# Kernel tuning notes

Hardware: AMD Instinct MI355X
Metric: run time of the kernel (lower is better)

Reference implementation:

```python
import jax, jax.numpy as jnp
import numpy as np

NUM_HEADS = 8
LN_EPS = 1e-5  # torch.nn.LayerNorm default


def setup_inputs() -> dict:
    key = jax.random.key(0)
    k1, k2, k3, k4 = jax.random.split(key, 4)
    B, S, H = 32, 512, 256
    inputs = jax.random.normal(k1, (B, S, H), dtype=jnp.float32)
    radial_mask = jax.random.uniform(k2, (B, S), dtype=jnp.float32, minval=1e-4, maxval=1.0)
    # torch Linear stores weight as [out, in]; init ~ U(-1/sqrt(in), 1/sqrt(in))
    bound = 1.0 / np.sqrt(H)
    in_proj_w = jax.random.uniform(k3, (3 * H, H), dtype=jnp.float32, minval=-bound, maxval=bound)
    out_proj_w = jax.random.uniform(k4, (H, H), dtype=jnp.float32, minval=-bound, maxval=bound)
    ln_gamma = jnp.ones((H,), dtype=jnp.float32)
    ln_beta = jnp.zeros((H,), dtype=jnp.float32)
    return {
        "inputs": inputs,
        "radial_mask": radial_mask,
        "in_proj_w": in_proj_w,
        "out_proj_w": out_proj_w,
        "ln_gamma": ln_gamma,
        "ln_beta": ln_beta,
    }


def reference(inputs, radial_mask, in_proj_w, out_proj_w, ln_gamma, ln_beta):
    B, S, H = inputs.shape
    nh = NUM_HEADS
    hd = H // nh

    # LayerNorm over the last dim
    mu = jnp.mean(inputs, axis=-1, keepdims=True)
    var = jnp.var(inputs, axis=-1, keepdims=True)
    normed = (inputs - mu) * jax.lax.rsqrt(var + LN_EPS) * ln_gamma + ln_beta

    # QKV projection (no bias); torch Linear: x @ W.T
    qkv = jnp.einsum('bsh,oh->bso', normed, in_proj_w)
    q, k, v = jnp.split(qkv, 3, axis=-1)

    # [B, S, H] -> [B, nh, S, hd]
    def to_heads(x):
        return x.reshape(B, S, nh, hd).transpose(0, 2, 1, 3)

    q = to_heads(q)
    k = to_heads(k)
    v = to_heads(v)

    # Custom transforms before SDPA
    q = q * q + 1e-6
    k = k + jnp.log(radial_mask)[:, None, :, None]

    # scaled_dot_product_attention with default scale = 1/sqrt(hd)
    scale = 1.0 / np.sqrt(hd).astype(np.float32)
    scores = jnp.einsum('bhqd,bhkd->bhqk', q, k) * scale
    attn = jax.nn.softmax(scores, axis=-1)
    out = jnp.einsum('bhqk,bhkd->bhqd', attn, v)

    # back to [B, S, H], output projection, residual with 1/sqrt(2)
    out = out.transpose(0, 2, 1, 3).reshape(B, S, H)
    out = jnp.einsum('bsh,oh->bso', out, out_proj_w)
    return (out + inputs) * np.float32(0.5 ** 0.5)
```

## Files before the change

kernel.cpp:

```cpp
#include <hip/hip_runtime.h>
#include <hip/hip_bf16.h>

typedef unsigned int u32;
typedef unsigned short u16;

#define B_   32
#define S_   512
#define H_   256
#define NH_  8
#define HD_  32

typedef __attribute__((ext_vector_type(8))) short short8;
typedef __attribute__((ext_vector_type(4))) float f32x4;

__device__ __forceinline__ float bfl(u32 u){ union{u32 i;float f;} c; c.i = u << 16;          return c.f; }
__device__ __forceinline__ float bfh(u32 u){ union{u32 i;float f;} c; c.i = u & 0xffff0000u;  return c.f; }
__device__ __forceinline__ float bf1(u16 u){ union{u32 i;float f;} c; c.i = ((u32)u) << 16;   return c.f; }
__device__ __forceinline__ u16   f2b(float f){ __hip_bfloat16 h = __float2bfloat16(f); return *reinterpret_cast<u16*>(&h); }
__device__ __forceinline__ u32   pk2(float a, float b){ return (u32)f2b(a) | ((u32)f2b(b) << 16); }
__device__ __forceinline__ void  unp8(const uint4 u, float* f){
  f[0]=bfl(u.x); f[1]=bfh(u.x); f[2]=bfl(u.y); f[3]=bfh(u.y);
  f[4]=bfl(u.z); f[5]=bfh(u.z); f[6]=bfl(u.w); f[7]=bfh(u.w);
}
__device__ __forceinline__ f32x4 mfma16(short8 a, short8 b, f32x4 c){
  return __builtin_amdgcn_mfma_f32_16x16x32_bf16(a, b, c, 0, 0, 0);
}

template<int F32>
__device__ __forceinline__ void load8(const void* p, int e8, float* f) {
  if (F32) {
    const float4* q = (const float4*)p;
    const float4 a = q[e8 * 2], b = q[e8 * 2 + 1];
    f[0]=a.x; f[1]=a.y; f[2]=a.z; f[3]=a.w; f[4]=b.x; f[5]=b.y; f[6]=b.z; f[7]=b.w;
  } else {
    unp8(((const uint4*)p)[e8], f);
  }
}
template<int F32>
__device__ __forceinline__ void store8(void* p, int e8, const float* f) {
  if (F32) {
    float4* q = (float4*)p;
    q[e8 * 2]     = make_float4(f[0], f[1], f[2], f[3]);
    q[e8 * 2 + 1] = make_float4(f[4], f[5], f[6], f[7]);
  } else {
    uint4 u;
    u.x = pk2(f[0], f[1]); u.y = pk2(f[2], f[3]);
    u.z = pk2(f[4], f[5]); u.w = pk2(f[6], f[7]);
    ((uint4*)p)[e8] = u;
  }
}
template<int F32>
__device__ __forceinline__ float load1(const void* p, size_t e) {
  return F32 ? ((const float*)p)[e] : bf1(((const u16*)p)[e]);
}
template<int F32>
__device__ __forceinline__ short8 loadBfrag(const void* wp, int row, int k0, int K) {
  if (F32) {
    const float* w = (const float*)wp + (size_t)row * K + k0;
    const float4 a = *(const float4*)w;
    const float4 b = *(const float4*)(w + 4);
    short8 r;
    r[0]=(short)f2b(a.x); r[1]=(short)f2b(a.y); r[2]=(short)f2b(a.z); r[3]=(short)f2b(a.w);
    r[4]=(short)f2b(b.x); r[5]=(short)f2b(b.y); r[6]=(short)f2b(b.z); r[7]=(short)f2b(b.w);
    return r;
  } else {
    return *(const short8*)((const u16*)wp + (size_t)row * K + k0);
  }
}

__device__ __forceinline__ int sniff_mode(const void* xin) {
  __shared__ int votes;
  const int tid = threadIdx.x;
  if (tid == 0) votes = 0;
  __syncthreads();
  const u32* xw = (const u32*)xin;
  int h = 0;
#pragma unroll
  for (int j = 0; j < 4; ++j) {
    const u32 u = xw[(tid << 2) + j];
    const u32 e = (u >> 7) & 0xFF;
    h += (e >= 100 && e <= 135) ? 1 : 0;
  }
  const unsigned long long m = __ballot(h >= 3);
  if ((tid & 63) == 0) atomicAdd(&votes, __popcll(m));
  __syncthreads();
  return (votes >= 128) ? 0 : 1;
}

template<int F32>
__global__ __launch_bounds__(256, 2) void ln_qkv_mfma(
    const void* __restrict__ xin, const void* __restrict__ rmask,
    const void* __restrict__ wi, const void* __restrict__ gamma,
    const void* __restrict__ beta,
    u16* __restrict__ qbuf, u16* __restrict__ kbuf, u16* __restrict__ vt)
{
  if (sniff_mode(xin) != F32) return;

  __shared__ __align__(16) u16 XnF[4 * 8 * 64 * 8];
  __shared__ float lmr[64];
  const int tid = threadIdx.x;
  const int l = tid & 63, w = tid >> 6;
  const int lr = l & 15, quad = l >> 4;
  const int row0 = (blockIdx.x >> 1) * 64;
  const int nhalf = blockIdx.x & 1;

  {
    const int r = tid >> 5, ln = tid & 31;
    float g[8], bb[8];
    load8<F32>(gamma, ln, g);
    load8<F32>(beta,  ln, bb);
    const int c = ln >> 2, qd = ln & 3;
#pragma unroll
    for (int p = 0; p < 8; ++p) {
      const int R = p * 8 + r;
      const int grow = row0 + R;
      float x[8]; load8<F32>(xin, grow * 32 + ln, x);
      float s = 0.f, sq = 0.f;
#pragma unroll
      for (int j = 0; j < 8; ++j) { s += x[j]; sq += x[j] * x[j]; }
#pragma unroll
      for (int m = 1; m < 32; m <<= 1) { s += __shfl_xor(s, m); sq += __shfl_xor(sq, m); }
      const float mu  = s * (1.f / 256.f);
      const float var = sq * (1.f / 256.f) - mu * mu;
      const float rs  = rsqrtf(var + 1e-5f);
      short8 pk;
#pragma unroll
      for (int j = 0; j < 8; ++j) pk[j] = (short)f2b((x[j] - mu) * rs * g[j] + bb[j]);
      const int t = R >> 4, rm = R & 15;
      *(short8*)(XnF + (((t * 8 + c) * 64 + qd * 16 + rm) << 3)) = pk;
      if (ln == 0) lmr[R] = logf(load1<F32>(rmask, grow));
    }
  }
  __syncthreads();

  short8 Af[4][8];
#pragma unroll
  for (int mt = 0; mt < 4; ++mt)
#pragma unroll
    for (int c = 0; c < 8; ++c)
      Af[mt][c] = *(const short8*)(XnF + (((mt * 8 + c) * 64 + l) << 3));

  const int bb_ = row0 >> 9;
  const int sB  = row0 & 511;
  const int tbase = nhalf * 24 + w * 6;

  short8 Bf[2][8];
#pragma unroll
  for (int c = 0; c < 8; ++c)
    Bf[0][c] = loadBfrag<F32>(wi, tbase * 16 + lr, c * 32 + quad * 8, 256);

#pragma unroll
  for (int nt = 0; nt < 6; ++nt) {
    const int cb = nt & 1;
    if (nt < 5) {
#pragma unroll
      for (int c = 0; c < 8; ++c)
        Bf[cb ^ 1][c] = loadBfrag<F32>(wi, (tbase + nt + 1) * 16 + lr, c * 32 + quad * 8, 256);
    }

    f32x4 a[4];
#pragma unroll
    for (int mt = 0; mt < 4; ++mt) a[mt] = (f32x4){0.f, 0.f, 0.f, 0.f};
#pragma unroll
    for (int c = 0; c < 8; ++c) {
#pragma unroll
      for (int mt = 0; mt < 4; ++mt)
        a[mt] = mfma16(Af[mt][c], Bf[cb][c], a[mt]);
    }

    const int nAbs  = (tbase + nt) * 16;
    const int type  = nAbs >> 8;
    const int dbase = nAbs & 255;
    if (type < 2) {
      const int d  = dbase + lr;
      const int h  = d >> 5, dd = d & 31;
      const int bh = bb_ * NH_ + h;
      u16* dst = (type == 0) ? qbuf : kbuf;
#pragma unroll
      for (int mt = 0; mt < 4; ++mt) {
        const int sL = mt * 16 + quad * 4;
#pragma unroll
        for (int i = 0; i < 4; ++i) {
          float v = a[mt][i];
          v = (type == 0) ? (v * v + 1e-6f) : (v + lmr[sL + i]);
          dst[((size_t)bh * S_ + sB + sL + i) * HD_ + dd] = f2b(v);
        }
      }
    } else {
      const int dv  = dbase + lr;
      const int hv  = dv >> 5, ddv = dv & 31;
      const int bhv = bb_ * NH_ + hv;
#pragma unroll
      for (int mt = 0; mt < 4; ++mt) {
        const int c16 = (sB >> 5) + (mt >> 1);
        const int slot16 = ((c16 * 2 + (ddv >> 4)) * 4 + quad) * 16 + (ddv & 15);
        uint2 pkv;
        pkv.x = pk2(a[mt][0], a[mt][1]);
        pkv.y = pk2(a[mt][2], a[mt][3]);
        *(uint2*)(vt + (size_t)bhv * (S_ * HD_) + slot16 * 8 + (mt & 1) * 4) = pkv;
      }
    }
  }
}

__global__ __launch_bounds__(256, 4) void attn_mfma(
    const u16* __restrict__ qbuf, const u16* __restrict__ kbuf,
    const u16* __restrict__ vt, u16* __restrict__ ctx)
{
  __shared__ __align__(16) u16 OB[4][16 * 40];
  const int tid = threadIdx.x;
  const int bh = blockIdx.x & 255, sq = blockIdx.x >> 8;
  const int l = tid & 63, w = tid >> 6;
  const int lr = l & 15, quad = l >> 4;
  const size_t kvbase = (size_t)bh * (S_ * HD_);
  const int q0 = sq * 64 + w * 16;

  const float cE = 0.17677669529663688f * 1.4426950408889634f;

  const short8 qf = *(const short8*)(qbuf + kvbase + (size_t)(q0 + lr) * HD_ + quad * 8);
  const u16* kp = kbuf + kvbase + (size_t)lr * HD_ + quad * 8;
  const u16* vp = vt + kvbase;

  float mS = -1e30f, lS = 0.f;
  f32x4 o0 = {0.f,0.f,0.f,0.f}, o1 = {0.f,0.f,0.f,0.f};

#pragma unroll
  for (int c = 0; c < 4; ++c) {
    f32x4 acc[8];
#pragma unroll
    for (int j = 0; j < 8; ++j) {
      const short8 kf = *(const short8*)(kp + (c * 8 + j) * (16 * HD_));
      f32x4 z = {0.f,0.f,0.f,0.f};
      acc[j] = mfma16(kf, qf, z);
    }

    float mc = acc[0][0];
#pragma unroll
    for (int j = 0; j < 8; ++j)
#pragma unroll
      for (int r = 0; r < 4; ++r) mc = fmaxf(mc, acc[j][r]);
    mc = fmaxf(mc, __shfl_xor(mc, 16));
    mc = fmaxf(mc, __shfl_xor(mc, 32));
    const float mNew  = fmaxf(mS, mc * cE);
    const float alpha = exp2f(mS - mNew);
    float sc = 0.f;
#pragma unroll
    for (int j = 0; j < 8; ++j)
#pragma unroll
      for (int r = 0; r < 4; ++r) {
        const float p = exp2f(fmaf(acc[j][r], cE, -mNew));
        acc[j][r] = p; sc += p;
      }
    sc += __shfl_xor(sc, 16);
    sc += __shfl_xor(sc, 32);
    lS = fmaf(lS, alpha, sc);
    mS = mNew;
#pragma unroll
    for (int r = 0; r < 4; ++r) { o0[r] *= alpha; o1[r] *= alpha; }

#pragma unroll
    for (int g = 0; g < 4; ++g) {
      union { u32 u[4]; short8 s; } pa;
      pa.u[0] = pk2(acc[2*g][0],   acc[2*g][1]);
      pa.u[1] = pk2(acc[2*g][2],   acc[2*g][3]);
      pa.u[2] = pk2(acc[2*g+1][0], acc[2*g+1][1]);
      pa.u[3] = pk2(acc[2*g+1][2], acc[2*g+1][3]);
      const int c16 = c * 4 + g;
      const short8 v0 = *(const short8*)(vp + (((c16 * 8 +     quad) * 16 + lr) << 3));
      const short8 v1 = *(const short8*)(vp + (((c16 * 8 + 4 + quad) * 16 + lr) << 3));
      o0 = mfma16(pa.s, v0, o0);
      o1 = mfma16(pa.s, v1, o1);
    }
  }
  const float inv = 1.f / lS;

  u16* ob = OB[w];
#pragma unroll
  for (int r = 0; r < 4; ++r) {
    const int qq = quad * 4 + r;
    const float iv = __shfl(inv, (l & 48) | qq);
    ob[qq * 40 + lr]      = f2b(o0[r] * iv);
    ob[qq * 40 + 16 + lr] = f2b(o1[r] * iv);
  }
  const uint4 ov = *(const uint4*)(ob + (l >> 2) * 40 + (l & 3) * 8);
  *(uint4*)(ctx + kvbase + (size_t)(q0 + (l >> 2)) * HD_ + (l & 3) * 8) = ov;
}

template<int F32>
__global__ __launch_bounds__(256) void proj_mfma(
    const u16* __restrict__ ctx, const void* __restrict__ xin,
    const void* __restrict__ wo, void* __restrict__ out)
{
  if (sniff_mode(xin) != F32) return;

  __shared__ __align__(16) u16 XnF[8 * 64 * 8];
  __shared__ __align__(16) u16 OutB[16 * 264];
  const int tid = threadIdx.x;
  const int l = tid & 63, w = tid >> 6;
  const int lr = l & 15, quad = l >> 4;
  const int row0 = blockIdx.x * 16;
  const int b = row0 >> 9, s0 = row0 & 511;

#pragma unroll
  for (int it = 0; it < 2; ++it) {
    const int idx = it * 256 + tid;
    const int dq = idx & 3, sl = (idx >> 2) & 15, h = idx >> 6;
    const uint4 cv = *(const uint4*)(ctx + ((size_t)(b * 8 + h) * S_ + s0 + sl) * HD_ + dq * 8);
    const int qds = dq ^ (sl & 3);
    *(uint4*)(XnF + ((h * 64 + qds * 16 + sl) << 3)) = cv;
  }
  __syncthreads();

  const int lsw = (quad ^ (lr & 3)) * 16 + lr;
  short8 Af[8];
#pragma unroll
  for (int c = 0; c < 8; ++c)
    Af[c] = *(const short8*)(XnF + ((c * 64 + lsw) << 3));

  short8 Bf[2][8];
#pragma unroll
  for (int c = 0; c < 8; ++c)
    Bf[0][c] = loadBfrag<F32>(wo, (w * 4) * 16 + lr, c * 32 + quad * 8, 256);

#pragma unroll
  for (int nt = 0; nt < 4; ++nt) {
    const int cb = nt & 1;
    if (nt < 3) {
#pragma unroll
      for (int c = 0; c < 8; ++c)
        Bf[cb ^ 1][c] = loadBfrag<F32>(wo, (w * 4 + nt + 1) * 16 + lr, c * 32 + quad * 8, 256);
    }
    const int n0 = (w * 4 + nt) * 16;
    f32x4 a0 = {0.f,0.f,0.f,0.f};
#pragma unroll
    for (int c = 0; c < 8; ++c)
      a0 = mfma16(Af[c], Bf[cb][c], a0);
#pragma unroll
    for (int i = 0; i < 4; ++i)
      OutB[(quad * 4 + i) * 264 + n0 + lr] = f2b(a0[i]);
  }
  __syncthreads();

  const int r  = tid >> 4;
  const int c8 = (tid & 15) * 2;
#pragma unroll
  for (int j8 = 0; j8 < 2; ++j8) {
    float xv[8]; load8<F32>(xin, (row0 + r) * 32 + c8 + j8, xv);
    float pv[8]; unp8(*(const uint4*)(OutB + r * 264 + (c8 + j8) * 8), pv);
    float ov[8];
#pragma unroll
    for (int j = 0; j < 8; ++j) ov[j] = (pv[j] + xv[j]) * 0.70710678f;
    store8<F32>(out, (row0 + r) * 32 + c8 + j8, ov);
  }
}

extern "C" void kernel_launch(void* const* d_in, const int* in_sizes, int n_in,
                              void* d_out, int out_size, void* d_ws, size_t ws_size,
                              hipStream_t stream)
{
  const void* xin   = d_in[0];
  const void* rmask = d_in[1];
  const void* wi    = d_in[2];
  const void* wo    = d_in[3];
  const void* gam   = d_in[4];
  const void* bet   = d_in[5];

  u16* q   = (u16*)d_ws;
  u16* k   = q + 4194304;
  u16* vt  = k + 4194304;
  u16* cxb = vt + 4194304;

  ln_qkv_mfma<0><<<512,  256, 0, stream>>>(xin, rmask, wi, gam, bet, q, k, vt);
  ln_qkv_mfma<1><<<512,  256, 0, stream>>>(xin, rmask, wi, gam, bet, q, k, vt);
  attn_mfma     <<<2048, 256, 0, stream>>>(q, k, vt, cxb);
  proj_mfma<0>  <<<1024, 256, 0, stream>>>(cxb, xin, wo, d_out);
  proj_mfma<1>  <<<1024, 256, 0, stream>>>(cxb, xin, wo, d_out);
}
```

Before: 181.0 us.

## Double per-wave query rows in attention and rows per block in output projection

The attention kernel now has each wave process two 16-row query tiles (32 rows), so every loaded K and V fragment feeds two sets of MFMAs, and the grid is halved. The output projection block now covers 32 rows instead of 16, reusing each loaded Wo fragment for two M-tiles, and its grid is also halved. This cuts redundant K/V and weight traffic per unit of work. In exchange it raises register pressure (the launch bounds are lowered to 3 and 2 waves) and leaves fewer blocks for latency hiding.

```diff
diff --git a/kernel.cpp b/kernel.cpp
--- a/kernel.cpp
+++ b/kernel.cpp
@@ -203,119 +203,143 @@
   }
 }
 
-__global__ __launch_bounds__(256, 4) void attn_mfma(
+__global__ __launch_bounds__(256, 3) void attn_mfma(
     const u16* __restrict__ qbuf, const u16* __restrict__ kbuf,
     const u16* __restrict__ vt, u16* __restrict__ ctx)
 {
-  __shared__ __align__(16) u16 OB[4][16 * 40];
+  __shared__ __align__(16) u16 OB[4][32 * 40];
   const int tid = threadIdx.x;
   const int bh = blockIdx.x & 255, sq = blockIdx.x >> 8;
   const int l = tid & 63, w = tid >> 6;
   const int lr = l & 15, quad = l >> 4;
   const size_t kvbase = (size_t)bh * (S_ * HD_);
-  const int q0 = sq * 64 + w * 16;
+  const int q0 = sq * 128 + w * 32;
 
   const float cE = 0.17677669529663688f * 1.4426950408889634f;
 
-  const short8 qf = *(const short8*)(qbuf + kvbase + (size_t)(q0 + lr) * HD_ + quad * 8);
+  const short8 qfA = *(const short8*)(qbuf + kvbase + (size_t)(q0 + lr) * HD_ + quad * 8);
+  const short8 qfB = *(const short8*)(qbuf + kvbase + (size_t)(q0 + 16 + lr) * HD_ + quad * 8);
   const u16* kp = kbuf + kvbase + (size_t)lr * HD_ + quad * 8;
   const u16* vp = vt + kvbase;
 
-  float mS = -1e30f, lS = 0.f;
-  f32x4 o0 = {0.f,0.f,0.f,0.f}, o1 = {0.f,0.f,0.f,0.f};
+  float mSA = -1e30f, lSA = 0.f, mSB = -1e30f, lSB = 0.f;
+  f32x4 oA0 = {0.f,0.f,0.f,0.f}, oA1 = {0.f,0.f,0.f,0.f};
+  f32x4 oB0 = {0.f,0.f,0.f,0.f}, oB1 = {0.f,0.f,0.f,0.f};
 
 #pragma unroll
   for (int c = 0; c < 4; ++c) {
-    f32x4 acc[8];
+    f32x4 aA[8], aB[8];
 #pragma unroll
     for (int j = 0; j < 8; ++j) {
       const short8 kf = *(const short8*)(kp + (c * 8 + j) * (16 * HD_));
       f32x4 z = {0.f,0.f,0.f,0.f};
-      acc[j] = mfma16(kf, qf, z);
-    }
-
-    float mc = acc[0][0];
+      aA[j] = mfma16(kf, qfA, z);
+      aB[j] = mfma16(kf, qfB, z);
+    }
+
+    float mcA = aA[0][0], mcB = aB[0][0];
 #pragma unroll
     for (int j = 0; j < 8; ++j)
 #pragma unroll
-      for (int r = 0; r < 4; ++r) mc = fmaxf(mc, acc[j][r]);
-    mc = fmaxf(mc, __shfl_xor(mc, 16));
-    mc = fmaxf(mc, __shfl_xor(mc, 32));
-    const float mNew  = fmaxf(mS, mc * cE);
-    const float alpha = exp2f(mS - mNew);
-    float sc = 0.f;
+      for (int r = 0; r < 4; ++r) { mcA = fmaxf(mcA, aA[j][r]); mcB = fmaxf(mcB, aB[j][r]); }
+    mcA = fmaxf(mcA, __shfl_xor(mcA, 16)); mcB = fmaxf(mcB, __shfl_xor(mcB, 16));
+    mcA = fmaxf(mcA, __shfl_xor(mcA, 32)); mcB = fmaxf(mcB, __shfl_xor(mcB, 32));
+    const float mNA = fmaxf(mSA, mcA * cE), mNB = fmaxf(mSB, mcB * cE);
+    const float alA = exp2f(mSA - mNA),     alB = exp2f(mSB - mNB);
+    float scA = 0.f, scB = 0.f;
 #pragma unroll
     for (int j = 0; j < 8; ++j)
 #pragma unroll
       for (int r = 0; r < 4; ++r) {
-        const float p = exp2f(fmaf(acc[j][r], cE, -mNew));
-        acc[j][r] = p; sc += p;
+        const float pA = exp2f(fmaf(aA[j][r], cE, -mNA));
+        const float pB = exp2f(fmaf(aB[j][r], cE, -mNB));
+        aA[j][r] = pA; scA += pA;
+        aB[j][r] = pB; scB += pB;
       }
-    sc += __shfl_xor(sc, 16);
-    sc += __shfl_xor(sc, 32);
-    lS = fmaf(lS, alpha, sc);
-    mS = mNew;
-#pragma unroll
-    for (int r = 0; r < 4; ++r) { o0[r] *= alpha; o1[r] *= alpha; }
+    scA += __shfl_xor(scA, 16); scB += __shfl_xor(scB, 16);
+    scA += __shfl_xor(scA, 32); scB += __shfl_xor(scB, 32);
+    lSA = fmaf(lSA, alA, scA); mSA = mNA;
+    lSB = fmaf(lSB, alB, scB); mSB = mNB;
+#pragma unroll
+    for (int r = 0; r < 4; ++r) {
+      oA0[r] *= alA; oA1[r] *= alA;
+      oB0[r] *= alB; oB1[r] *= alB;
+    }
 
 #pragma unroll
     for (int g = 0; g < 4; ++g) {
-      union { u32 u[4]; short8 s; } pa;
-      pa.u[0] = pk2(acc[2*g][0],   acc[2*g][1]);
-      pa.u[1] = pk2(acc[2*g][2],   acc[2*g][3]);
-      pa.u[2] = pk2(acc[2*g+1][0], acc[2*g+1][1]);
-      pa.u[3] = pk2(acc[2*g+1][2], acc[2*g+1][3]);
       const int c16 = c * 4 + g;
       const short8 v0 = *(const short8*)(vp + (((c16 * 8 +     quad) * 16 + lr) << 3));
       const short8 v1 = *(const short8*)(vp + (((c16 * 8 + 4 + quad) * 16 + lr) << 3));
-      o0 = mfma16(pa.s, v0, o0);
-      o1 = mfma16(pa.s, v1, o1);
-    }
-  }
-  const float inv = 1.f / lS;
+      union { u32 u[4]; short8 s; } pa;
+      pa.u[0] = pk2(aA[2*g][0],   aA[2*g][1]);
+      pa.u[1] = pk2(aA[2*g][2],   aA[2*g][3]);
+      pa.u[2] = pk2(aA[2*g+1][0], aA[2*g+1][1]);
+      pa.u[3] = pk2(aA[2*g+1][2], aA[2*g+1][3]);
+      oA0 = mfma16(pa.s, v0, oA0);
+      oA1 = mfma16(pa.s, v1, oA1);
+      pa.u[0] = pk2(aB[2*g][0],   aB[2*g][1]);
+      pa.u[1] = pk2(aB[2*g][2],   aB[2*g][3]);
+      pa.u[2] = pk2(aB[2*g+1][0], aB[2*g+1][1]);
+      pa.u[3] = pk2(aB[2*g+1][2], aB[2*g+1][3]);
+      oB0 = mfma16(pa.s, v0, oB0);
+      oB1 = mfma16(pa.s, v1, oB1);
+    }
+  }
+  const float invA = 1.f / lSA, invB = 1.f / lSB;
 
   u16* ob = OB[w];
 #pragma unroll
   for (int r = 0; r < 4; ++r) {
     const int qq = quad * 4 + r;
-    const float iv = __shfl(inv, (l & 48) | qq);
-    ob[qq * 40 + lr]      = f2b(o0[r] * iv);
-    ob[qq * 40 + 16 + lr] = f2b(o1[r] * iv);
-  }
-  const uint4 ov = *(const uint4*)(ob + (l >> 2) * 40 + (l & 3) * 8);
-  *(uint4*)(ctx + kvbase + (size_t)(q0 + (l >> 2)) * HD_ + (l & 3) * 8) = ov;
-}
-
-template<int F32>
-__global__ __launch_bounds__(256) void proj_mfma(
+    const float ivA = __shfl(invA, (l & 48) | qq);
+    const float ivB = __shfl(invB, (l & 48) | qq);
+    ob[qq * 40 + lr]             = f2b(oA0[r] * ivA);
+    ob[qq * 40 + 16 + lr]        = f2b(oA1[r] * ivA);
+    ob[(16 + qq) * 40 + lr]      = f2b(oB0[r] * ivB);
+    ob[(16 + qq) * 40 + 16 + lr] = f2b(oB1[r] * ivB);
+  }
+#pragma unroll
+  for (int t = 0; t < 2; ++t) {
+    const int row = (l >> 2) + t * 16;
+    const uint4 ov = *(const uint4*)(ob + row * 40 + (l & 3) * 8);
+    *(uint4*)(ctx + kvbase + (size_t)(q0 + row) * HD_ + (l & 3) * 8) = ov;
+  }
+}
+
+template<int F32>
+__global__ __launch_bounds__(256, 2) void proj_mfma(
     const u16* __restrict__ ctx, const void* __restrict__ xin,
     const void* __restrict__ wo, void* __restrict__ out)
 {
   if (sniff_mode(xin) != F32) return;
 
-  __shared__ __align__(16) u16 XnF[8 * 64 * 8];
-  __shared__ __align__(16) u16 OutB[16 * 264];
+  __shared__ __align__(16) u16 XnF[2 * 8 * 64 * 8];
+  __shared__ __align__(16) u16 OutB[32 * 264];
   const int tid = threadIdx.x;
   const int l = tid & 63, w = tid >> 6;
   const int lr = l & 15, quad = l >> 4;
-  const int row0 = blockIdx.x * 16;
+  const int row0 = blockIdx.x * 32;
   const int b = row0 >> 9, s0 = row0 & 511;
 
 #pragma unroll
-  for (int it = 0; it < 2; ++it) {
+  for (int it = 0; it < 4; ++it) {
     const int idx = it * 256 + tid;
-    const int dq = idx & 3, sl = (idx >> 2) & 15, h = idx >> 6;
+    const int dq = idx & 3, sl = (idx >> 2) & 31, h = idx >> 7;
     const uint4 cv = *(const uint4*)(ctx + ((size_t)(b * 8 + h) * S_ + s0 + sl) * HD_ + dq * 8);
-    const int qds = dq ^ (sl & 3);
-    *(uint4*)(XnF + ((h * 64 + qds * 16 + sl) << 3)) = cv;
+    const int t = sl >> 4, rm = sl & 15;
+    const int qds = dq ^ (rm & 3);
+    *(uint4*)(XnF + (((t * 8 + h) * 64 + qds * 16 + rm) << 3)) = cv;
   }
   __syncthreads();
 
   const int lsw = (quad ^ (lr & 3)) * 16 + lr;
-  short8 Af[8];
-#pragma unroll
-  for (int c = 0; c < 8; ++c)
-    Af[c] = *(const short8*)(XnF + ((c * 64 + lsw) << 3));
+  short8 Af[2][8];
+#pragma unroll
+  for (int mt = 0; mt < 2; ++mt)
+#pragma unroll
+    for (int c = 0; c < 8; ++c)
+      Af[mt][c] = *(const short8*)(XnF + (((mt * 8 + c) * 64 + lsw) << 3));
 
   short8 Bf[2][8];
 #pragma unroll
@@ -331,20 +355,26 @@
         Bf[cb ^ 1][c] = loadBfrag<F32>(wo, (w * 4 + nt + 1) * 16 + lr, c * 32 + quad * 8, 256);
     }
     const int n0 = (w * 4 + nt) * 16;
-    f32x4 a0 = {0.f,0.f,0.f,0.f};
-#pragma unroll
-    for (int c = 0; c < 8; ++c)
-      a0 = mfma16(Af[c], Bf[cb][c], a0);
-#pragma unroll
-    for (int i = 0; i < 4; ++i)
-      OutB[(quad * 4 + i) * 264 + n0 + lr] = f2b(a0[i]);
+    f32x4 a0 = {0.f,0.f,0.f,0.f}, a1 = {0.f,0.f,0.f,0.f};
+#pragma unroll
+    for (int c = 0; c < 8; ++c) {
+      a0 = mfma16(Af[0][c], Bf[cb][c], a0);
+      a1 = mfma16(Af[1][c], Bf[cb][c], a1);
+    }
+#pragma unroll
+    for (int m = 0; m < 2; ++m) {
+      const f32x4 acc = m ? a1 : a0;
+#pragma unroll
+      for (int i = 0; i < 4; ++i)
+        OutB[(m * 16 + quad * 4 + i) * 264 + n0 + lr] = f2b(acc[i]);
+    }
   }
   __syncthreads();
 
-  const int r  = tid >> 4;
-  const int c8 = (tid & 15) * 2;
-#pragma unroll
-  for (int j8 = 0; j8 < 2; ++j8) {
+  const int r  = tid >> 3;
+  const int c8 = (tid & 7) * 4;
+#pragma unroll
+  for (int j8 = 0; j8 < 4; ++j8) {
     float xv[8]; load8<F32>(xin, (row0 + r) * 32 + c8 + j8, xv);
     float pv[8]; unp8(*(const uint4*)(OutB + r * 264 + (c8 + j8) * 8), pv);
     float ov[8];
@@ -372,7 +402,7 @@
 
   ln_qkv_mfma<0><<<512,  256, 0, stream>>>(xin, rmask, wi, gam, bet, q, k, vt);
   ln_qkv_mfma<1><<<512,  256, 0, stream>>>(xin, rmask, wi, gam, bet, q, k, vt);
-  attn_mfma     <<<2048, 256, 0, stream>>>(q, k, vt, cxb);
-  proj_mfma<0>  <<<1024, 256, 0, stream>>>(cxb, xin, wo, d_out);
-  proj_mfma<1>  <<<1024, 256, 0, stream>>>(cxb, xin, wo, d_out);
-}
+  attn_mfma     <<<1024, 256, 0, stream>>>(q, k, vt, cxb);
+  proj_mfma<0>  <<<512,  256, 0, stream>>>(cxb, xin, wo, d_out);
+  proj_mfma<1>  <<<512,  256, 0, stream>>>(cxb, xin, wo, d_out);
+}
```

After: 167.8 us. 7.3% less time.
